# Optimization experiments

Hardware: AMD Instinct MI355X
Metric: run time of the kernel (lower is better)

The kernel has to match this reference:

```python
import jax, jax.numpy as jnp
import numpy as np

N_ATOM, N_CHI, N_BOND, N_DIR = 119, 3, 5, 3
NUM_LAYER, EMB, FEAT, NG = 5, 300, 256, 4096
N_NODES, N_EDGES = 100000, 200000


def setup_inputs() -> dict:
    key = jax.random.key(0)
    ks = jax.random.split(key, 16)
    N, E = N_NODES, N_EDGES
    r = lambda k, s, sc: jax.random.normal(k, s, jnp.float32) * sc
    inp = {}
    inp["atom_type"] = jax.random.randint(ks[0], (N,), 0, N_ATOM, dtype=jnp.int32)
    inp["chirality"] = jax.random.randint(ks[1], (N,), 0, N_CHI, dtype=jnp.int32)
    inp["edge_index"] = jax.random.randint(ks[2], (2, E), 0, N, dtype=jnp.int32)
    inp["edge_type"] = jax.random.randint(ks[3], (E,), 0, 4, dtype=jnp.int32)
    inp["edge_dir"] = jax.random.randint(ks[4], (E,), 0, N_DIR, dtype=jnp.int32)
    inp["batch"] = jnp.sort(jax.random.randint(ks[5], (N,), 0, NG, dtype=jnp.int32))
    inp["atom_emb1"] = r(ks[6], (N_ATOM, EMB), 0.02)
    inp["atom_emb2"] = r(ks[7], (N_CHI, EMB), 0.02)
    inp["W"] = r(ks[8], (NUM_LAYER, EMB, EMB), 0.05)
    inp["b"] = jnp.zeros((NUM_LAYER, EMB), jnp.float32)
    inp["ee1"] = r(ks[9], (NUM_LAYER, N_BOND, 1), 0.5)
    inp["ee2"] = r(ks[10], (NUM_LAYER, N_DIR, 1), 0.5)
    inp["bn_gamma"] = jnp.ones((NUM_LAYER, EMB), jnp.float32)
    inp["bn_beta"] = jnp.zeros((NUM_LAYER, EMB), jnp.float32)
    inp["feat_W"] = r(ks[11], (EMB, FEAT), 0.05)
    inp["feat_b"] = jnp.zeros((FEAT,), jnp.float32)
    inp["head_W1"] = r(ks[12], (FEAT, FEAT // 2), 0.08)
    inp["head_b1"] = jnp.zeros((FEAT // 2,), jnp.float32)
    inp["head_W2"] = r(ks[13], (FEAT // 2, 2), 0.1)
    inp["head_b2"] = jnp.zeros((2,), jnp.float32)
    return inp


def reference(atom_type, chirality, edge_index, edge_type, edge_dir, batch,
              atom_emb1, atom_emb2, W, b, ee1, ee2, bn_gamma, bn_beta,
              feat_W, feat_b, head_W1, head_b1, head_W2, head_b2):
    N = atom_type.shape[0]
    # add self loops (edge_attr: bond_type=4, direction=0)
    loops = jnp.arange(N, dtype=edge_index.dtype)
    row = jnp.concatenate([edge_index[0], loops])
    col = jnp.concatenate([edge_index[1], loops])
    et = jnp.concatenate([edge_type, jnp.full((N,), 4, edge_type.dtype)])
    ed = jnp.concatenate([edge_dir, jnp.zeros((N,), edge_dir.dtype)])

    h = atom_emb1[atom_type] + atom_emb2[chirality]  # [N, EMB]
    for l in range(NUM_LAYER):
        hx = h @ W[l]                                  # [N, EMB]
        edge_emb = ee1[l][et] + ee2[l][ed]             # [E+N, 1]
        msg = hx[row] + edge_emb                       # gather + broadcast add
        out = jax.ops.segment_sum(msg, col, num_segments=N) + b[l]
        # BatchNorm1d (training-mode batch stats, eps=1e-5)
        mean = out.mean(axis=0)
        var = out.var(axis=0)
        h = bn_gamma[l] * (out - mean) * jax.lax.rsqrt(var + 1e-5) + bn_beta[l]
        if l < NUM_LAYER - 1:
            h = jax.nn.relu(h)  # drop_ratio=0 -> dropout is identity

    # global mean pool over graphs
    sums = jax.ops.segment_sum(h, batch, num_segments=NG)              # [NG, EMB]
    counts = jax.ops.segment_sum(jnp.ones((N, 1), h.dtype), batch, num_segments=NG)
    hg = sums / jnp.maximum(counts, 1.0)

    hf = hg @ feat_W + feat_b                                          # [NG, FEAT]
    pred = jax.nn.softplus(hf @ head_W1 + head_b1) @ head_W2 + head_b2  # [NG, 2]
    return hf, pred
```

## Files before the change

kernel.cpp:

```cpp
#include <hip/hip_runtime.h>
#include <math.h>

typedef unsigned short u16;
typedef unsigned int u32;
typedef short v8s __attribute__((ext_vector_type(8)));
typedef float v4f __attribute__((ext_vector_type(4)));

#define EMB 300
#define SP 320
#define NGRP 4096
#define FEAT 256
#define MT 128
#define NT 160
#define NCOMB 357
#define NREP 32
#define CSB (NREP * 2 * SP)

__device__ __forceinline__ u16 f2bf(float x) {
    u32 u = __float_as_uint(x);
    u += 0x7FFFu + ((u >> 16) & 1u);
    return (u16)(u >> 16);
}
__device__ __forceinline__ float bf2f(u16 h) {
    return __uint_as_float((u32)h << 16);
}
__device__ __forceinline__ void unpack8(uint4 w, float* o) {
    const u32* p = &w.x;
#pragma unroll
    for (int q = 0; q < 4; q++) {
        o[2 * q]     = __uint_as_float(p[q] << 16);
        o[2 * q + 1] = __uint_as_float(p[q] & 0xFFFF0000u);
    }
}
__device__ __forceinline__ v8s clampA(uint4 w, float4 ta, float4 tb) {
    const u32* p = &w.x;
    float t[8] = {ta.x, ta.y, ta.z, ta.w, tb.x, tb.y, tb.z, tb.w};
    u32 o[4];
#pragma unroll
    for (int q = 0; q < 4; q++) {
        float lo = __uint_as_float(p[q] << 16);
        float hi = __uint_as_float(p[q] & 0xFFFF0000u);
        lo = fmaxf(lo, t[2 * q]);
        hi = fmaxf(hi, t[2 * q + 1]);
        o[q] = (__float_as_uint(lo) >> 16) | (__float_as_uint(hi) & 0xFFFF0000u);
    }
    uint4 r = make_uint4(o[0], o[1], o[2], o[3]);
    return *(v8s*)&r;
}
__device__ __forceinline__ void dma16(const u16* g, u16* l) {
    __builtin_amdgcn_global_load_lds(
        (const __attribute__((address_space(1))) unsigned int*)g,
        (__attribute__((address_space(3))) unsigned int*)l, 16, 0, 0);
}

__global__ void k_prep_n(const int* __restrict__ at, const int* __restrict__ ch,
                         int* __restrict__ c9, int* __restrict__ deg,
                         int* __restrict__ cursor, float* __restrict__ cs0,
                         u16* __restrict__ Q, int N) {
    int n = blockIdx.x * blockDim.x + threadIdx.x;
    if (n < N) {
        c9[n] = at[n] * 3 + ch[n];
        deg[n] = 0;
        cursor[n] = 0;
    }
    if (n < CSB) cs0[n] = 0.f;
    if (n < SP / 2) ((u32*)(Q + (size_t)N * SP))[n] = 0u;
}

__global__ void k_count(const int* __restrict__ col, int* __restrict__ deg, int E) {
    int e = blockIdx.x * blockDim.x + threadIdx.x;
    if (e < E) atomicAdd(&deg[col[e]], 1);
}

__global__ __launch_bounds__(256) void k_bsum(const int* __restrict__ deg,
                                              int* __restrict__ bsum, int N) {
    int base = blockIdx.x * 1024 + threadIdx.x * 4;
    int s = 0;
    if (base + 3 < N) {
        int4 v = *(const int4*)(deg + base);
        s = v.x + v.y + v.z + v.w;
    } else {
        for (int j = 0; j < 4; j++) if (base + j < N) s += deg[base + j];
    }
    __shared__ int red[256];
    red[threadIdx.x] = s;
    __syncthreads();
    for (int off = 128; off > 0; off >>= 1) {
        if (threadIdx.x < off) red[threadIdx.x] += red[threadIdx.x + off];
        __syncthreads();
    }
    if (threadIdx.x == 0) bsum[blockIdx.x] = red[0];
}

__global__ __launch_bounds__(128) void k_scanb(const int* __restrict__ bsum,
                                               int* __restrict__ boff, int NB) {
    __shared__ int sh[128];
    int t = threadIdx.x;
    int v = (t < NB) ? bsum[t] : 0;
    sh[t] = v;
    __syncthreads();
    for (int off = 1; off < 128; off <<= 1) {
        int add = (t >= off) ? sh[t - off] : 0;
        __syncthreads();
        sh[t] += add;
        __syncthreads();
    }
    if (t < NB) boff[t] = sh[t] - v;
}

__global__ __launch_bounds__(256) void k_indptr(const int* __restrict__ deg,
                                                const int* __restrict__ boff,
                                                int* __restrict__ indptr, int N) {
    int b = blockIdx.x, t = threadIdx.x;
    int base = b * 1024 + t * 4;
    int v[4] = {0, 0, 0, 0};
    if (base + 3 < N) {
        int4 w = *(const int4*)(deg + base);
        v[0] = w.x; v[1] = w.y; v[2] = w.z; v[3] = w.w;
    } else {
        for (int j = 0; j < 4; j++) if (base + j < N) v[j] = deg[base + j];
    }
    int tsum = v[0] + v[1] + v[2] + v[3];
    __shared__ int sh[256];
    sh[t] = tsum;
    __syncthreads();
    for (int off = 1; off < 256; off <<= 1) {
        int add = (t >= off) ? sh[t - off] : 0;
        __syncthreads();
        sh[t] += add;
        __syncthreads();
    }
    int run = boff[b] + sh[t] - tsum;
    for (int j = 0; j < 4; j++) {
        run += v[j];
        if (base + j < N) indptr[base + j + 1] = run;
    }
    if (b == 0 && t == 0) indptr[0] = 0;
}

__global__ void k_fill(const int* __restrict__ row, const int* __restrict__ col,
                       const int* __restrict__ et, const int* __restrict__ ed,
                       const int* __restrict__ indptr, int* __restrict__ cursor,
                       int* __restrict__ packed, int E) {
    int e = blockIdx.x * blockDim.x + threadIdx.x;
    if (e >= E) return;
    int c = col[e];
    int pos = indptr[c] + atomicAdd(&cursor[c], 1);
    packed[pos] = row[e] | ((et[e] * 3 + ed[e]) << 17);
}

__global__ void k_comb(const float* __restrict__ e1, const float* __restrict__ e2,
                       u16* __restrict__ comb) {
    int idx = blockIdx.x * blockDim.x + threadIdx.x;
    if (idx >= NCOMB * 40) return;
    int row = idx / 40, f = idx % 40;
    int at = row / 3, ch = row % 3;
    u32 o[4];
#pragma unroll
    for (int q = 0; q < 4; q++) {
        int c0 = f * 8 + q * 2;
        float x0 = 0.f, x1 = 0.f;
        if (c0 < EMB)     x0 = e1[(size_t)at * EMB + c0] + e2[(size_t)ch * EMB + c0];
        if (c0 + 1 < EMB) x1 = e1[(size_t)at * EMB + c0 + 1] + e2[(size_t)ch * EMB + c0 + 1];
        o[q] = (u32)f2bf(x0) | ((u32)f2bf(x1) << 16);
    }
    *(uint4*)(comb + (size_t)row * SP + f * 8) = make_uint4(o[0], o[1], o[2], o[3]);
}

__global__ __launch_bounds__(320) void k_wprep(
    const float* __restrict__ Wl, const float* __restrict__ cs,
    const float* __restrict__ gamma, const float* __restrict__ beta,
    int ident, int N, u16* __restrict__ Wt, float* __restrict__ srow,
    float* __restrict__ thr) {
    __shared__ float wred[5];
    int n = blockIdx.x;
    int k = threadIdx.x;
    float scv, shv, thv;
    if (ident) {
        scv = (k < EMB) ? 1.f : 0.f;
        shv = 0.f;
        thv = -__builtin_inff();
    } else if (k < EMB) {
        float s1 = 0.f, s2 = 0.f;
        for (int r = 0; r < NREP; r++) {
            s1 += cs[r * 2 * SP + k];
            s2 += cs[r * 2 * SP + SP + k];
        }
        float inv = 1.f / (float)N;
        float mean = s1 * inv;
        float var = s2 * inv - mean * mean;
        float rstd = rsqrtf(fmaxf(var, 0.f) + 1e-5f);
        scv = gamma[k] * rstd;
        shv = beta[k] - mean * scv;
        thv = bf2f(f2bf(-shv / scv));
    } else {
        scv = 0.f; shv = 0.f; thv = -__builtin_inff();
    }
    if (n == 0) thr[k] = thv;

    float w = 0.f;
    if (n < EMB && k < EMB) w = Wl[(size_t)k * EMB + n];
    Wt[(size_t)n * SP + k] = f2bf(w * scv);
    float s = (k < EMB) ? shv * w : 0.f;
#pragma unroll
    for (int o2 = 32; o2 > 0; o2 >>= 1) s += __shfl_down(s, o2);
    if ((k & 63) == 0) wred[k >> 6] = s;
    __syncthreads();
    if (k == 0) {
        float t = wred[0] + wred[1] + wred[2] + wred[3] + wred[4];
        srow[n] = (n < EMB) ? t : 0.f;
    }
}

__global__ void k_finalize(const float* __restrict__ cs,
                           const float* __restrict__ gamma, const float* __restrict__ beta,
                           float* __restrict__ sc, float* __restrict__ sh, int N) {
    int c = threadIdx.x;
    if (c >= SP) return;
    float s1 = 0.f, s2 = 0.f;
    for (int r = 0; r < NREP; r++) {
        s1 += cs[r * 2 * SP + c];
        s2 += cs[r * 2 * SP + SP + c];
    }
    if (c < EMB) {
        float inv = 1.f / (float)N;
        float mean = s1 * inv;
        float var = s2 * inv - mean * mean;
        float rstd = rsqrtf(fmaxf(var, 0.f) + 1e-5f);
        float s = gamma[c] * rstd;
        sc[c] = s;
        sh[c] = beta[c] - mean * s;
    } else {
        sc[c] = 0.f; sh[c] = 0.f;
    }
}

__global__ __launch_bounds__(256) void k_gemm(
    const u16* __restrict__ A, const u16* __restrict__ Wt,
    const float* __restrict__ thr, const float* __restrict__ srow,
    u16* __restrict__ C, int M, const int* __restrict__ rowmap,
    float* __restrict__ zbank) {
    __shared__ __align__(16) u16 sm[18432];

    int m0 = blockIdx.y * MT;
    int n0 = blockIdx.x * NT;
    int tid = threadIdx.x;
    int wave = tid >> 6, lane = tid & 63;
    int wm = wave >> 1, wn = wave & 1;
    int lm = lane & 15, quad = lane >> 4;

    if (blockIdx.x == 0 && blockIdx.y == 0)
        for (int i = tid; i < CSB; i += 256) zbank[i] = 0.f;

    int ar0 = min(m0 + (tid >> 2), M - 1);
    int ar1 = min(m0 + 64 + (tid >> 2), M - 1);
    if (rowmap) { ar0 = rowmap[ar0]; ar1 = rowmap[ar1]; }
    const u16* ag0 = A + (size_t)ar0 * SP + (tid & 3) * 8;
    const u16* ag1 = A + (size_t)ar1 * SP + (tid & 3) * 8;
    const u16* bg0 = Wt + (size_t)(n0 + (tid >> 2)) * SP + (tid & 3) * 8;
    const u16* bg1 = Wt + (size_t)(n0 + 64 + (tid >> 2)) * SP + (tid & 3) * 8;
    const u16* bg2 = Wt + (size_t)(n0 + 128 + (tid >> 2)) * SP + (tid & 3) * 8;

    const float* tp = thr + quad * 8;

    v4f acc[4][5];
#pragma unroll
    for (int nf = 0; nf < 5; nf++) {
        float sv = srow[n0 + wn * 80 + nf * 16 + lm];
#pragma unroll
        for (int mf = 0; mf < 4; mf++)
            acc[mf][nf] = (v4f){sv, sv, sv, sv};
    }

    auto issue = [&](int d, int kt) {
        int ko = kt * 32;
        u16* ad = sm + d * 4096;
        u16* bd = sm + 8192 + d * 5120;
        dma16(ag0 + ko, ad + tid * 8);
        dma16(ag1 + ko, ad + (256 + tid) * 8);
        dma16(bg0 + ko, bd + tid * 8);
        dma16(bg1 + ko, bd + (256 + tid) * 8);
        if (tid < 128) dma16(bg2 + ko, bd + (512 + tid) * 8);
    };

    issue(0, 0);
    for (int kt = 0; kt < SP / 32; kt++) {
        __syncthreads();
        if (kt + 1 < SP / 32) issue((kt + 1) & 1, kt + 1);
        const u16* as = sm + (kt & 1) * 4096;
        const u16* bs = sm + 8192 + (kt & 1) * 5120;
        float4 ta = *(const float4*)(tp + kt * 32);
        float4 tb = *(const float4*)(tp + kt * 32 + 4);
        v8s b[5], a[4];
#pragma unroll
        for (int nf = 0; nf < 5; nf++)
            b[nf] = *(const v8s*)(bs + (wn * 80 + nf * 16 + lm) * 32 + quad * 8);
#pragma unroll
        for (int mf = 0; mf < 4; mf++) {
            uint4 w = *(const uint4*)(as + (wm * 64 + mf * 16 + lm) * 32 + quad * 8);
            a[mf] = clampA(w, ta, tb);
        }
#pragma unroll
        for (int nf = 0; nf < 5; nf++)
#pragma unroll
            for (int mf = 0; mf < 4; mf++)
                acc[mf][nf] = __builtin_amdgcn_mfma_f32_16x16x32_bf16(a[mf], b[nf], acc[mf][nf], 0, 0, 0);
    }

    __syncthreads();
#pragma unroll
    for (int p = 0; p < 2; p++) {
#pragma unroll
        for (int mf2 = 0; mf2 < 2; mf2++) {
            int mf = p * 2 + mf2;
#pragma unroll
            for (int nf = 0; nf < 5; nf++)
#pragma unroll
                for (int r = 0; r < 4; r++)
                    sm[(wm * 32 + mf2 * 16 + quad * 4 + r) * 168 + wn * 80 + nf * 16 + lm] =
                        f2bf(acc[mf][nf][r]);
        }
        __syncthreads();
#pragma unroll
        for (int i = 0; i < 5; i++) {
            int slot = tid + i * 256;
            int lr = slot / 20, cg = slot % 20;
            int grow = m0 + (lr >> 5) * 64 + p * 32 + (lr & 31);
            if (grow < M)
                *(uint4*)(C + (size_t)grow * SP + n0 + cg * 8) =
                    *(const uint4*)(sm + lr * 168 + cg * 8);
        }
        __syncthreads();
    }
}

__global__ __launch_bounds__(320) void k_aggf(
    const u16* __restrict__ Q, const int* __restrict__ indptr,
    const int* __restrict__ packed, const float* __restrict__ e1,
    const float* __restrict__ e2, u16* __restrict__ P,
    float* __restrict__ colstats, int N) {
    __shared__ float tab[16];
    __shared__ float part[8][328];
    int tid = threadIdx.x;
    int f = tid % 40;
    int slot = tid / 40;
    int n = blockIdx.x * 8 + slot;
    int nn = min(n, N - 1);

    uint4 sg = *(const uint4*)(Q + (size_t)nn * SP + f * 8);
    int i = indptr[nn];
    int e = indptr[nn + 1];

    if (tid < 16) tab[tid] = (tid < 15) ? e1[tid / 3] + e2[tid % 3] : 0.f;
    __syncthreads();

    float psum[8] = {0, 0, 0, 0, 0, 0, 0, 0};
    float psq[8]  = {0, 0, 0, 0, 0, 0, 0, 0};

    if (n < N) {
        const int PKZ = N | (15 << 17);
        float acc[8];
        unpack8(sg, acc);
        float s = tab[12];
        while (i < e) {
            int pk0 = packed[i];
            int pk1 = (i + 1 < e) ? packed[i + 1] : PKZ;
            int pk2 = (i + 2 < e) ? packed[i + 2] : PKZ;
            int pk3 = (i + 3 < e) ? packed[i + 3] : PKZ;
            uint4 g0 = *(const uint4*)(Q + (size_t)(pk0 & 0x1FFFF) * SP + f * 8);
            uint4 g1 = *(const uint4*)(Q + (size_t)(pk1 & 0x1FFFF) * SP + f * 8);
            uint4 g2 = *(const uint4*)(Q + (size_t)(pk2 & 0x1FFFF) * SP + f * 8);
            uint4 g3 = *(const uint4*)(Q + (size_t)(pk3 & 0x1FFFF) * SP + f * 8);
            float t[8];
            unpack8(g0, t);
#pragma unroll
            for (int q = 0; q < 8; q++) acc[q] += t[q];
            unpack8(g1, t);
#pragma unroll
            for (int q = 0; q < 8; q++) acc[q] += t[q];
            unpack8(g2, t);
#pragma unroll
            for (int q = 0; q < 8; q++) acc[q] += t[q];
            unpack8(g3, t);
#pragma unroll
            for (int q = 0; q < 8; q++) acc[q] += t[q];
            s += tab[pk0 >> 17] + tab[pk1 >> 17] + tab[pk2 >> 17] + tab[pk3 >> 17];
            i += 4;
        }
        u32 o[4];
#pragma unroll
        for (int q = 0; q < 4; q++) {
            float r0 = acc[2 * q] + s;
            float r1 = acc[2 * q + 1] + s;
            psum[2 * q] = r0;      psum[2 * q + 1] = r1;
            psq[2 * q]  = r0 * r0; psq[2 * q + 1]  = r1 * r1;
            o[q] = (u32)f2bf(r0) | ((u32)f2bf(r1) << 16);
        }
        *(uint4*)(P + (size_t)n * SP + f * 8) = make_uint4(o[0], o[1], o[2], o[3]);
    }

    int rep = (blockIdx.x & (NREP - 1)) * 2 * SP;
#pragma unroll
    for (int j = 0; j < 8; j++) part[slot][f * 8 + j] = psum[j];
    __syncthreads();
    {
        float s = 0.f;
#pragma unroll
        for (int k = 0; k < 8; k++) s += part[k][tid];
        atomicAdd(&colstats[rep + tid], s);
    }
    __syncthreads();
#pragma unroll
    for (int j = 0; j < 8; j++) part[slot][f * 8 + j] = psq[j];
    __syncthreads();
    {
        float s = 0.f;
#pragma unroll
        for (int k = 0; k < 8; k++) s += part[k][tid];
        atomicAdd(&colstats[rep + SP + tid], s);
    }
}

__global__ void k_bounds(const int* __restrict__ batch, int* __restrict__ gstart, int N) {
    int n = blockIdx.x * blockDim.x + threadIdx.x;
    if (n > N) return;
    int bcur = (n < N) ? batch[n] : NGRP;
    int bprev = (n > 0) ? batch[n - 1] : -1;
    for (int g = bprev + 1; g <= bcur; g++) gstart[g] = n;
}

__global__ __launch_bounds__(320) void k_pool(
    const u16* __restrict__ P, const float* __restrict__ sc,
    const float* __restrict__ sh, const int* __restrict__ gstart,
    float* __restrict__ hg) {
    int tid = threadIdx.x;
    int g = blockIdx.x * 8 + tid / 40;
    int f = tid % 40;
    int r0 = gstart[g], r1 = gstart[g + 1];
    int cnt = r1 - r0;
    float acc[8] = {0, 0, 0, 0, 0, 0, 0, 0};
    for (int r = r0; r < r1; r++) {
        float t[8];
        unpack8(*(const uint4*)(P + (size_t)r * SP + f * 8), t);
#pragma unroll
        for (int j = 0; j < 8; j++) acc[j] += t[j];
    }
    float inv = 1.f / (float)max(cnt, 1);
#pragma unroll
    for (int j = 0; j < 8; j++) {
        int c = f * 8 + j;
        if (c < EMB)
            hg[(size_t)g * EMB + c] = (acc[j] * sc[c] + (float)cnt * sh[c]) * inv;
    }
}

__global__ __launch_bounds__(256) void k_feat(const float* __restrict__ hg,
                                              const float* __restrict__ fW,
                                              const float* __restrict__ fb,
                                              float* __restrict__ hf) {
    __shared__ float hgs[16 * EMB];
    int g0 = blockIdx.x * 16;
    int tid = threadIdx.x;
    for (int i = tid; i < 16 * EMB; i += 256) {
        int gi = i / EMB, c = i % EMB;
        hgs[i] = hg[(size_t)(g0 + gi) * EMB + c];
    }
    __syncthreads();
    float acc[16];
    float fbv = fb[tid];
#pragma unroll
    for (int gi = 0; gi < 16; gi++) acc[gi] = fbv;
    for (int k = 0; k < EMB; k++) {
        float w = fW[(size_t)k * FEAT + tid];
#pragma unroll
        for (int gi = 0; gi < 16; gi++) acc[gi] += hgs[gi * EMB + k] * w;
    }
#pragma unroll
    for (int gi = 0; gi < 16; gi++) hf[(size_t)(g0 + gi) * FEAT + tid] = acc[gi];
}

__global__ __launch_bounds__(128) void k_head(const float* __restrict__ hf,
                                              const float* __restrict__ W1,
                                              const float* __restrict__ b1,
                                              const float* __restrict__ W2,
                                              const float* __restrict__ b2,
                                              float* __restrict__ pred) {
    __shared__ float hfs[8 * FEAT];
    __shared__ float sred[2][8][2];
    int g0 = blockIdx.x * 8;
    int tid = threadIdx.x;
    for (int i = tid; i < 8 * FEAT; i += 128) {
        int gi = i >> 8, k = i & 255;
        hfs[i] = hf[(size_t)(g0 + gi) * FEAT + k];
    }
    __syncthreads();
    float acc[8];
    float b1v = b1[tid];
#pragma unroll
    for (int gi = 0; gi < 8; gi++) acc[gi] = b1v;
    for (int k = 0; k < FEAT; k++) {
        float w = W1[(size_t)k * 128 + tid];
#pragma unroll
        for (int gi = 0; gi < 8; gi++) acc[gi] += hfs[gi * FEAT + k] * w;
    }
    float w20 = W2[tid * 2], w21 = W2[tid * 2 + 1];
    int wv = tid >> 6;
#pragma unroll
    for (int gi = 0; gi < 8; gi++) {
        float x = acc[gi];
        float t = fmaxf(x, 0.f) + log1pf(expf(-fabsf(x)));
        float p0 = t * w20, p1 = t * w21;
#pragma unroll
        for (int off = 32; off > 0; off >>= 1) {
            p0 += __shfl_down(p0, off);
            p1 += __shfl_down(p1, off);
        }
        if ((tid & 63) == 0) { sred[wv][gi][0] = p0; sred[wv][gi][1] = p1; }
    }
    __syncthreads();
    if (tid < 16) {
        int gi = tid >> 1, o = tid & 1;
        pred[(size_t)(g0 + gi) * 2 + o] = sred[0][gi][o] + sred[1][gi][o] + b2[o];
    }
}

extern "C" void kernel_launch(void* const* d_in, const int* in_sizes, int n_in,
                              void* d_out, int out_size, void* d_ws, size_t ws_size,
                              hipStream_t stream) {
    const int* atom_type = (const int*)d_in[0];
    const int* chir      = (const int*)d_in[1];
    const int* eidx      = (const int*)d_in[2];
    const int* etype     = (const int*)d_in[3];
    const int* edir      = (const int*)d_in[4];
    const int* batch     = (const int*)d_in[5];
    const float* emb1    = (const float*)d_in[6];
    const float* emb2    = (const float*)d_in[7];
    const float* W       = (const float*)d_in[8];
    const float* ee1     = (const float*)d_in[10];
    const float* ee2     = (const float*)d_in[11];
    const float* gamma   = (const float*)d_in[12];
    const float* beta    = (const float*)d_in[13];
    const float* featW   = (const float*)d_in[14];
    const float* featb   = (const float*)d_in[15];
    const float* hW1     = (const float*)d_in[16];
    const float* hb1     = (const float*)d_in[17];
    const float* hW2     = (const float*)d_in[18];
    const float* hb2     = (const float*)d_in[19];

    int N = in_sizes[0];
    int E = in_sizes[2] / 2;
    const int* erow = eidx;
    const int* ecol = eidx + E;

    size_t off = 0;
    char* base = (char*)d_ws;
    auto carve = [&](size_t bytes) -> void* {
        void* p = base + off;
        off += (bytes + 255) & ~(size_t)255;
        return p;
    };
    u16*   P        = (u16*)  carve((size_t)(N + 1) * SP * 2);
    u16*   Q        = (u16*)  carve((size_t)(N + 1) * SP * 2);
    u16*   Wt       = (u16*)  carve((size_t)SP * SP * 2);
    u16*   comb     = (u16*)  carve((size_t)NCOMB * SP * 2);
    int*   c9map    = (int*)  carve((size_t)N * 4);
    int*   deg      = (int*)  carve((size_t)N * 4);
    int*   cursor   = (int*)  carve((size_t)N * 4);
    int*   indptr   = (int*)  carve((size_t)(N + 1) * 4);
    int*   packed   = (int*)  carve((size_t)(E + 8) * 4);
    int*   bsum     = (int*)  carve(1024 * 4);
    int*   boff     = (int*)  carve(1024 * 4);
    float* cs0      = (float*)carve((size_t)CSB * 4);
    float* cs1      = (float*)carve((size_t)CSB * 4);
    float* scale_bn = (float*)carve(SP * 4);
    float* shift_bn = (float*)carve(SP * 4);
    float* thr_bn   = (float*)carve(SP * 4);
    float* srow     = (float*)carve(SP * 4);
    int*   gstart   = (int*)  carve((size_t)(NGRP + 1) * 4);
    float* hg       = (float*)carve((size_t)NGRP * EMB * 4);

    float* hf   = (float*)d_out;
    float* pred = (float*)d_out + (size_t)NGRP * FEAT;

    int eb = (E + 255) / 256;
    int NB = (N + 1023) / 1024;
    k_prep_n<<<(N + 255) / 256, 256, 0, stream>>>(atom_type, chir, c9map, deg, cursor,
                                                  cs0, Q, N);
    k_count<<<eb, 256, 0, stream>>>(ecol, deg, E);
    k_bsum<<<NB, 256, 0, stream>>>(deg, bsum, N);
    k_scanb<<<1, 128, 0, stream>>>(bsum, boff, NB);
    k_indptr<<<NB, 256, 0, stream>>>(deg, boff, indptr, N);
    k_fill<<<eb, 256, 0, stream>>>(erow, ecol, etype, edir, indptr, cursor, packed, E);

    k_comb<<<(NCOMB * 40 + 255) / 256, 256, 0, stream>>>(emb1, emb2, comb);

    dim3 ggrid(2, (N + MT - 1) / MT);
    int ab = (N + 7) / 8;
    float* banks[2] = {cs0, cs1};
    for (int l = 0; l < 5; l++) {
        float* wb = banks[l & 1];
        float* rb = banks[(l + 1) & 1];
        k_wprep<<<SP, 320, 0, stream>>>(W + (size_t)l * EMB * EMB, rb,
                                        gamma + l * EMB - EMB, beta + l * EMB - EMB,
                                        l == 0 ? 1 : 0, N, Wt, srow, thr_bn);
        if (l == 0)
            k_gemm<<<ggrid, 256, 0, stream>>>(comb, Wt, thr_bn, srow, Q, N, c9map, wb);
        else
            k_gemm<<<ggrid, 256, 0, stream>>>(P, Wt, thr_bn, srow, Q, N, nullptr, wb);
        k_aggf<<<ab, 320, 0, stream>>>(Q, indptr, packed, ee1 + l * 5, ee2 + l * 3, P,
                                       wb, N);
    }

    k_finalize<<<1, SP, 0, stream>>>(banks[4 & 1], gamma + 4 * EMB, beta + 4 * EMB,
                                     scale_bn, shift_bn, N);
    k_bounds<<<(N + 1 + 255) / 256, 256, 0, stream>>>(batch, gstart, N);
    k_pool<<<NGRP / 8, 320, 0, stream>>>(P, scale_bn, shift_bn, gstart, hg);
    k_feat<<<NGRP / 16, 256, 0, stream>>>(hg, featW, featb, hf);
    k_head<<<NGRP / 8, 128, 0, stream>>>(hf, hW1, hb1, hW2, hb2, pred);
}
```

Baseline: 691.4 us.

## Load A tiles through registers, clamp once at staging, skip clamp on layer 0

The GEMM now loads A tiles into registers two steps ahead, applies the ReLU/BN threshold clamp once per element while storing into LDS, and drops the per-wave clamp at fragment read time. Previously each element was clamped redundantly by both column-halves of waves. Thresholds are cached in shared memory, layer 0 skips the clamp entirely, and the bf16 packing uses a byte-permute instruction. The cost is losing the asynchronous global-to-LDS DMA for A, so register pressure and explicit load latency may rise.

```diff
diff --git a/kernel.cpp b/kernel.cpp
--- a/kernel.cpp
+++ b/kernel.cpp
@@ -32,7 +32,7 @@
         o[2 * q + 1] = __uint_as_float(p[q] & 0xFFFF0000u);
     }
 }
-__device__ __forceinline__ v8s clampA(uint4 w, float4 ta, float4 tb) {
+__device__ __forceinline__ uint4 clamp4(uint4 w, float4 ta, float4 tb) {
     const u32* p = &w.x;
     float t[8] = {ta.x, ta.y, ta.z, ta.w, tb.x, tb.y, tb.z, tb.w};
     u32 o[4];
@@ -42,10 +42,10 @@
         float hi = __uint_as_float(p[q] & 0xFFFF0000u);
         lo = fmaxf(lo, t[2 * q]);
         hi = fmaxf(hi, t[2 * q + 1]);
-        o[q] = (__float_as_uint(lo) >> 16) | (__float_as_uint(hi) & 0xFFFF0000u);
-    }
-    uint4 r = make_uint4(o[0], o[1], o[2], o[3]);
-    return *(v8s*)&r;
+        o[q] = __builtin_amdgcn_perm(__float_as_uint(hi), __float_as_uint(lo),
+                                     0x07060302u);
+    }
+    return make_uint4(o[0], o[1], o[2], o[3]);
 }
 __device__ __forceinline__ void dma16(const u16* g, u16* l) {
     __builtin_amdgcn_global_load_lds(
@@ -239,8 +239,9 @@
     const u16* __restrict__ A, const u16* __restrict__ Wt,
     const float* __restrict__ thr, const float* __restrict__ srow,
     u16* __restrict__ C, int M, const int* __restrict__ rowmap,
-    float* __restrict__ zbank) {
+    float* __restrict__ zbank, int doclamp) {
     __shared__ __align__(16) u16 sm[18432];
+    __shared__ float thrs[SP];
 
     int m0 = blockIdx.y * MT;
     int n0 = blockIdx.x * NT;
@@ -251,6 +252,8 @@
 
     if (blockIdx.x == 0 && blockIdx.y == 0)
         for (int i = tid; i < CSB; i += 256) zbank[i] = 0.f;
+
+    for (int i = tid; i < SP; i += 256) thrs[i] = thr[i];
 
     int ar0 = min(m0 + (tid >> 2), M - 1);
     int ar1 = min(m0 + 64 + (tid >> 2), M - 1);
@@ -261,8 +264,6 @@
     const u16* bg1 = Wt + (size_t)(n0 + 64 + (tid >> 2)) * SP + (tid & 3) * 8;
     const u16* bg2 = Wt + (size_t)(n0 + 128 + (tid >> 2)) * SP + (tid & 3) * 8;
 
-    const float* tp = thr + quad * 8;
-
     v4f acc[4][5];
 #pragma unroll
     for (int nf = 0; nf < 5; nf++) {
@@ -272,34 +273,52 @@
             acc[mf][nf] = (v4f){sv, sv, sv, sv};
     }
 
-    auto issue = [&](int d, int kt) {
+    auto issueB = [&](int d, int kt) {
         int ko = kt * 32;
-        u16* ad = sm + d * 4096;
         u16* bd = sm + 8192 + d * 5120;
-        dma16(ag0 + ko, ad + tid * 8);
-        dma16(ag1 + ko, ad + (256 + tid) * 8);
         dma16(bg0 + ko, bd + tid * 8);
         dma16(bg1 + ko, bd + (256 + tid) * 8);
         if (tid < 128) dma16(bg2 + ko, bd + (512 + tid) * 8);
     };
-
-    issue(0, 0);
+    auto stageA = [&](int d, int kt, uint4 r0, uint4 r1) {
+        u16* ad = sm + d * 4096;
+        if (doclamp) {
+            float4 t0 = *(const float4*)(thrs + kt * 32 + (tid & 3) * 8);
+            float4 t1 = *(const float4*)(thrs + kt * 32 + (tid & 3) * 8 + 4);
+            r0 = clamp4(r0, t0, t1);
+            r1 = clamp4(r1, t0, t1);
+        }
+        *(uint4*)(ad + tid * 8) = r0;
+        *(uint4*)(ad + (256 + tid) * 8) = r1;
+    };
+
+    uint4 ra0 = *(const uint4*)(ag0);
+    uint4 ra1 = *(const uint4*)(ag1);
+    issueB(0, 0);
+    __syncthreads();
+    stageA(0, 0, ra0, ra1);
+    ra0 = *(const uint4*)(ag0 + 32);
+    ra1 = *(const uint4*)(ag1 + 32);
+
     for (int kt = 0; kt < SP / 32; kt++) {
         __syncthreads();
-        if (kt + 1 < SP / 32) issue((kt + 1) & 1, kt + 1);
+        if (kt + 1 < SP / 32) {
+            issueB((kt + 1) & 1, kt + 1);
+            stageA((kt + 1) & 1, kt + 1, ra0, ra1);
+        }
+        if (kt + 2 < SP / 32) {
+            ra0 = *(const uint4*)(ag0 + (kt + 2) * 32);
+            ra1 = *(const uint4*)(ag1 + (kt + 2) * 32);
+        }
         const u16* as = sm + (kt & 1) * 4096;
         const u16* bs = sm + 8192 + (kt & 1) * 5120;
-        float4 ta = *(const float4*)(tp + kt * 32);
-        float4 tb = *(const float4*)(tp + kt * 32 + 4);
         v8s b[5], a[4];
 #pragma unroll
         for (int nf = 0; nf < 5; nf++)
             b[nf] = *(const v8s*)(bs + (wn * 80 + nf * 16 + lm) * 32 + quad * 8);
 #pragma unroll
-        for (int mf = 0; mf < 4; mf++) {
-            uint4 w = *(const uint4*)(as + (wm * 64 + mf * 16 + lm) * 32 + quad * 8);
-            a[mf] = clampA(w, ta, tb);
-        }
+        for (int mf = 0; mf < 4; mf++)
+            a[mf] = *(const v8s*)(as + (wm * 64 + mf * 16 + lm) * 32 + quad * 8);
 #pragma unroll
         for (int nf = 0; nf < 5; nf++)
 #pragma unroll
@@ -604,9 +623,9 @@
                                         gamma + l * EMB - EMB, beta + l * EMB - EMB,
                                         l == 0 ? 1 : 0, N, Wt, srow, thr_bn);
         if (l == 0)
-            k_gemm<<<ggrid, 256, 0, stream>>>(comb, Wt, thr_bn, srow, Q, N, c9map, wb);
+            k_gemm<<<ggrid, 256, 0, stream>>>(comb, Wt, thr_bn, srow, Q, N, c9map, wb, 0);
         else
-            k_gemm<<<ggrid, 256, 0, stream>>>(P, Wt, thr_bn, srow, Q, N, nullptr, wb);
+            k_gemm<<<ggrid, 256, 0, stream>>>(P, Wt, thr_bn, srow, Q, N, nullptr, wb, 1);
         k_aggf<<<ab, 320, 0, stream>>>(Q, indptr, packed, ee1 + l * 5, ee2 + l * 3, P,
                                        wb, N);
     }
```

New measurement: 697.0 us. About the same (+0.8%).

## Double GEMM K-tile to 64 with swizzled B layout and LDS thresholds

Applied to the files above, without the earlier changes.

The GEMM main loop now stages 64-wide K tiles per barrier instead of 32, halving the number of sync/issue iterations. The B tile uses a 64-column LDS layout with an XOR swizzle on odd rows to avoid bank conflicts, and threshold values are cached in LDS. The bf16 pack in the clamp is replaced by a single byte-permute instruction. LDS use roughly doubles, which may reduce occupancy.

```diff
diff --git a/kernel.cpp b/kernel.cpp
--- a/kernel.cpp
+++ b/kernel.cpp
@@ -42,7 +42,8 @@
         float hi = __uint_as_float(p[q] & 0xFFFF0000u);
         lo = fmaxf(lo, t[2 * q]);
         hi = fmaxf(hi, t[2 * q + 1]);
-        o[q] = (__float_as_uint(lo) >> 16) | (__float_as_uint(hi) & 0xFFFF0000u);
+        o[q] = __builtin_amdgcn_perm(__float_as_uint(hi), __float_as_uint(lo),
+                                     0x07060302u);
     }
     uint4 r = make_uint4(o[0], o[1], o[2], o[3]);
     return *(v8s*)&r;
@@ -240,7 +241,8 @@
     const float* __restrict__ thr, const float* __restrict__ srow,
     u16* __restrict__ C, int M, const int* __restrict__ rowmap,
     float* __restrict__ zbank) {
-    __shared__ __align__(16) u16 sm[18432];
+    __shared__ __align__(16) u16 sm[36864];
+    __shared__ float thrs[SP];
 
     int m0 = blockIdx.y * MT;
     int n0 = blockIdx.x * NT;
@@ -252,16 +254,16 @@
     if (blockIdx.x == 0 && blockIdx.y == 0)
         for (int i = tid; i < CSB; i += 256) zbank[i] = 0.f;
 
+    for (int i = tid; i < SP; i += 256) thrs[i] = thr[i];
+
     int ar0 = min(m0 + (tid >> 2), M - 1);
     int ar1 = min(m0 + 64 + (tid >> 2), M - 1);
     if (rowmap) { ar0 = rowmap[ar0]; ar1 = rowmap[ar1]; }
     const u16* ag0 = A + (size_t)ar0 * SP + (tid & 3) * 8;
     const u16* ag1 = A + (size_t)ar1 * SP + (tid & 3) * 8;
-    const u16* bg0 = Wt + (size_t)(n0 + (tid >> 2)) * SP + (tid & 3) * 8;
-    const u16* bg1 = Wt + (size_t)(n0 + 64 + (tid >> 2)) * SP + (tid & 3) * 8;
-    const u16* bg2 = Wt + (size_t)(n0 + 128 + (tid >> 2)) * SP + (tid & 3) * 8;
-
-    const float* tp = thr + quad * 8;
+    int rb = tid >> 3;
+    int cb = (tid & 7) ^ ((rb & 1) << 2);
+    const u16* bgs = Wt + (size_t)(n0 + rb) * SP + cb * 8;
 
     v4f acc[4][5];
 #pragma unroll
@@ -273,38 +275,48 @@
     }
 
     auto issue = [&](int d, int kt) {
-        int ko = kt * 32;
-        u16* ad = sm + d * 4096;
-        u16* bd = sm + 8192 + d * 5120;
-        dma16(ag0 + ko, ad + tid * 8);
-        dma16(ag1 + ko, ad + (256 + tid) * 8);
-        dma16(bg0 + ko, bd + tid * 8);
-        dma16(bg1 + ko, bd + (256 + tid) * 8);
-        if (tid < 128) dma16(bg2 + ko, bd + (512 + tid) * 8);
+        int ko = kt * 64;
+        u16* ad = sm + d * 8192;
+        u16* bd = sm + 16384 + d * 10240;
+        dma16(ag0 + ko,      ad + tid * 8);
+        dma16(ag1 + ko,      ad + (256 + tid) * 8);
+        dma16(ag0 + ko + 32, ad + (512 + tid) * 8);
+        dma16(ag1 + ko + 32, ad + (768 + tid) * 8);
+#pragma unroll
+        for (int j = 0; j < 5; j++)
+            dma16(bgs + (size_t)(32 * j) * SP + ko, bd + (j * 256 + tid) * 8);
     };
 
     issue(0, 0);
-    for (int kt = 0; kt < SP / 32; kt++) {
-        __syncthreads();
-        if (kt + 1 < SP / 32) issue((kt + 1) & 1, kt + 1);
-        const u16* as = sm + (kt & 1) * 4096;
-        const u16* bs = sm + 8192 + (kt & 1) * 5120;
-        float4 ta = *(const float4*)(tp + kt * 32);
-        float4 tb = *(const float4*)(tp + kt * 32 + 4);
-        v8s b[5], a[4];
-#pragma unroll
-        for (int nf = 0; nf < 5; nf++)
-            b[nf] = *(const v8s*)(bs + (wn * 80 + nf * 16 + lm) * 32 + quad * 8);
-#pragma unroll
-        for (int mf = 0; mf < 4; mf++) {
-            uint4 w = *(const uint4*)(as + (wm * 64 + mf * 16 + lm) * 32 + quad * 8);
-            a[mf] = clampA(w, ta, tb);
+    for (int kt = 0; kt < SP / 64; kt++) {
+        __syncthreads();
+        if (kt + 1 < SP / 64) issue((kt + 1) & 1, kt + 1);
+        const u16* as = sm + (kt & 1) * 8192;
+        const u16* bs = sm + 16384 + (kt & 1) * 10240;
+#pragma unroll
+        for (int kk = 0; kk < 2; kk++) {
+            float4 ta = *(const float4*)(thrs + kt * 64 + kk * 32 + quad * 8);
+            float4 tb = *(const float4*)(thrs + kt * 64 + kk * 32 + quad * 8 + 4);
+            v8s b[5], a[4];
+#pragma unroll
+            for (int nf = 0; nf < 5; nf++) {
+                int row = wn * 80 + nf * 16 + lm;
+                b[nf] = *(const v8s*)(bs + row * 64 +
+                                      ((kk * 32 + quad * 8) ^ ((row & 1) << 5)));
+            }
+#pragma unroll
+            for (int mf = 0; mf < 4; mf++) {
+                uint4 w = *(const uint4*)(as + kk * 4096 +
+                                          (wm * 64 + mf * 16 + lm) * 32 + quad * 8);
+                a[mf] = clampA(w, ta, tb);
+            }
+#pragma unroll
+            for (int nf = 0; nf < 5; nf++)
+#pragma unroll
+                for (int mf = 0; mf < 4; mf++)
+                    acc[mf][nf] = __builtin_amdgcn_mfma_f32_16x16x32_bf16(
+                        a[mf], b[nf], acc[mf][nf], 0, 0, 0);
         }
-#pragma unroll
-        for (int nf = 0; nf < 5; nf++)
-#pragma unroll
-            for (int mf = 0; mf < 4; mf++)
-                acc[mf][nf] = __builtin_amdgcn_mfma_f32_16x16x32_bf16(a[mf], b[nf], acc[mf][nf], 0, 0, 0);
     }
 
     __syncthreads();
```

Result: slower. 717.1 us (+3.7%).
